# Performance work log

Measured on AMD Instinct MI355X. Metric: run time of the kernel, lower is better.

The kernel has to match this reference:

```python
import jax, jax.numpy as jnp
import numpy as np

EPS_XVAR = 1e-06
EPS_QVAR = 1e-05
EPS_VAR = 1e-05
MIN_SCALE = 0.1  # rbf kernel
EPS_EDGE = 1e-06


def setup_inputs() -> dict:
    key = jax.random.key(0)
    k1, k2, k3, k4 = jax.random.split(key, 4)
    B, O, I, M = 2048, 64, 64, 32
    x = jax.random.normal(k1, (B, I), dtype=jnp.float32)
    # inducing locations: linspace(-1.5, 1.5, M) tiled over (O, I)
    z = jnp.broadcast_to(jnp.linspace(-1.5, 1.5, M, dtype=jnp.float32), (O, I, M))
    q_mu = jax.random.normal(k2, (O, I, M), dtype=jnp.float32) * 0.05
    q_log_var = jnp.full((O, I, M), -3.0, dtype=jnp.float32)
    log_scale = jnp.zeros((O, I), dtype=jnp.float32)
    log_variance = jnp.full((O, I), -1.0, dtype=jnp.float32)
    return {"x": x, "z": z, "q_mu": q_mu, "q_log_var": q_log_var,
            "log_scale": log_scale, "log_variance": log_variance}


def reference(x, z, q_mu, q_log_var, log_scale, log_variance):
    # x: [B, I]; params: [O, I, M] or [O, I]
    x_mean = x
    x_var = jnp.zeros_like(x) + EPS_XVAR

    q_var = jnp.maximum(jnp.exp(q_log_var), EPS_QVAR)           # [O, I, M]
    var_kern = jnp.maximum(jnp.exp(log_variance), EPS_VAR)      # [O, I]
    lengthscale = jnp.maximum(jnp.exp(log_scale), MIN_SCALE)    # [O, I]

    x_mu_exp = x_mean[:, None, :, None]        # [B, 1, I, 1]
    x_var_exp = x_var[:, None, :, None]        # [B, 1, I, 1]
    ell_sq = (lengthscale ** 2)[None, :, :, None]  # [1, O, I, 1]
    vk = var_kern[None, :, :, None]            # [1, O, I, 1]

    denom = ell_sq + x_var_exp                 # [B, O, I, 1]
    diff = x_mu_exp - z[None]                  # [B, O, I, M]
    psi_1 = vk * jnp.sqrt(ell_sq / denom) * jnp.exp(-0.5 * diff ** 2 / denom)

    edge_means = jnp.sum(psi_1 * q_mu[None], axis=-1)                      # [B, O, I]
    edge_vars = jnp.sum(psi_1 ** 2 * (q_var + q_mu ** 2)[None], axis=-1)   # [B, O, I]
    edge_vars = jnp.maximum(edge_vars - edge_means ** 2, EPS_EDGE)

    return edge_means.sum(axis=2), edge_vars.sum(axis=2)  # each [B, O]
```

## Files before the change

kernel.cpp:

```cpp
#include <hip/hip_runtime.h>

#define BATCH 2048
#define ODIM 64
#define IDIM 64
#define MDIM 32

static constexpr float LOG2E = 1.4426950408889634f;

#if __has_builtin(__builtin_amdgcn_exp2f)
#define EXP2F(x) __builtin_amdgcn_exp2f(x)
#else
#define EXP2F(x) exp2f(x)
#endif

typedef float v2f __attribute__((ext_vector_type(2)));


__global__ __launch_bounds__(256) void prep_kernel(
    const float* __restrict__ z, const float* __restrict__ q_mu,
    const float* __restrict__ q_log_var, const float* __restrict__ log_scale,
    const float* __restrict__ log_variance,
    float4* __restrict__ cmq, float4* __restrict__ aux)
{
    int qt = blockIdx.x * 256 + threadIdx.x;
    int oi = qt >> 4;
    int k  = qt & 15;
    int g  = oi * MDIM + 2 * k;

    float ls   = log_scale[oi];
    float lv   = log_variance[oi];
    float ell  = fmaxf(expf(ls), 0.1f);
    float ell2 = ell * ell;
    float vk   = fmaxf(expf(lv), 1e-5f);
    float denom = ell2 + 1e-6f;
    float A    = vk * sqrtf(ell2 / denom);
    float a    = -0.5f * LOG2E / denom;

    float qm0 = q_mu[g],     qm1 = q_mu[g + 1];
    float qv0 = fmaxf(expf(q_log_var[g]),     1e-5f);
    float qv1 = fmaxf(expf(q_log_var[g + 1]), 1e-5f);
    float zm0 = z[g],        zm1 = z[g + 1];
    float w0  = exp2f(a * zm0 * zm0);
    float w1  = exp2f(a * zm1 * zm1);

    float4 c;
    c.x = A * qm0 * w0;
    c.y = A * A * (qv0 + qm0 * qm0) * w0 * w0;
    c.z = A * qm1 * w1;
    c.w = A * A * (qv1 + qm1 * qm1) * w1 * w1;
    cmq[qt] = c;

    if (k == 0) {
        float z0 = z[oi * MDIM + 0];
        float z1 = z[oi * MDIM + 1];
        float dz = z1 - z0;
        aux[oi] = make_float4(a, -2.0f * a * z0, -2.0f * a * dz, 0.0f);
    }
}

__global__ __launch_bounds__(512, 8) void gpkan_main_kernel(
    const float* __restrict__ x, const float4* __restrict__ cmq,
    const float4* __restrict__ aux, float* __restrict__ out)
{
    const int o     = blockIdx.x & (ODIM - 1);
    const int btile = blockIdx.x >> 6;
    const int tid   = threadIdx.x;
    const int lane  = tid & 63;
    const int wave  = __builtin_amdgcn_readfirstlane(tid >> 6);
    const int b0    = btile * 128 + 2 * lane;
    const int i0    = wave * 8;

    __shared__ float red[2][8][128];

    const float4* pA = (const float4*)(x + (size_t)b0 * IDIM + i0);
    const float4* pB = (const float4*)(x + (size_t)(b0 + 1) * IDIM + i0);
    float4 a0 = pA[0], a1 = pA[1];
    float4 bb0 = pB[0], bb1 = pB[1];

    v2f xv[8];
    xv[0].x = a0.x; xv[0].y = bb0.x;
    xv[1].x = a0.y; xv[1].y = bb0.y;
    xv[2].x = a0.z; xv[2].y = bb0.z;
    xv[3].x = a0.w; xv[3].y = bb0.w;
    xv[4].x = a1.x; xv[4].y = bb1.x;
    xv[5].x = a1.y; xv[5].y = bb1.y;
    xv[6].x = a1.z; xv[6].y = bb1.z;
    xv[7].x = a1.w; xv[7].y = bb1.w;

    const float4* __restrict__ Cb = cmq + ((size_t)o * IDIM + i0) * 16;
    const float4* __restrict__ Ab = aux + o * IDIM + i0;

    v2f emt = {0.f, 0.f};
    v2f evt = {0.f, 0.f};

    #pragma unroll
    for (int ii = 0; ii < 8; ++ii) {
        const float4 Ax = Ab[ii];
        const v2f x2 = xv[ii];

        v2f e1 = {Ax.x, Ax.x}, e2 = {Ax.y, Ax.y}, rc = {Ax.z, Ax.z};

        v2f t = __builtin_elementwise_fma(e1, x2, e2) * x2;
        v2f Eb;
        Eb.x = EXP2F(t.x); Eb.y = EXP2F(t.y);
        v2f ur = rc * x2;
        v2f rr;
        rr.x = EXP2F(ur.x); rr.y = EXP2F(ur.y);

        v2f s = rr * rr;
        v2f u = s * s;

        v2f Pe = {0.f, 0.f}, Po = {0.f, 0.f};
        v2f Qe = {0.f, 0.f}, Qo = {0.f, 0.f};

        const float4* C = Cb + ii * 16;
        #pragma unroll
        for (int k = 15; k >= 0; --k) {
            float4 c = C[k];
            v2f c1e = {c.x, c.x}, c2e = {c.y, c.y};
            v2f c1o = {c.z, c.z}, c2o = {c.w, c.w};
            Pe = __builtin_elementwise_fma(Pe, s, c1e);
            Po = __builtin_elementwise_fma(Po, s, c1o);
            Qe = __builtin_elementwise_fma(Qe, u, c2e);
            Qo = __builtin_elementwise_fma(Qo, u, c2o);
        }

        v2f P = __builtin_elementwise_fma(rr, Po, Pe);
        v2f Q = __builtin_elementwise_fma(s,  Qo, Qe);

        v2f em_i = Eb * P;
        v2f ev_i = (Eb * Eb) * Q;

        v2f eps = {1e-6f, 1e-6f};
        v2f d   = __builtin_elementwise_fma(-em_i, em_i, ev_i);
        evt += __builtin_elementwise_max(d, eps);
        emt += em_i;
    }

    red[0][wave][2 * lane + 0] = emt.x;
    red[0][wave][2 * lane + 1] = emt.y;
    red[1][wave][2 * lane + 0] = evt.x;
    red[1][wave][2 * lane + 1] = evt.y;
    __syncthreads();

    if (tid < 256) {
        const int sel = tid >> 7;
        const int l   = tid & 127;
        float acc = 0.f;
        #pragma unroll
        for (int w = 0; w < 8; ++w) acc += red[sel][w][l];
        const int bb = btile * 128 + l;
        if (sel == 0) out[bb * ODIM + o] = acc;
        else          out[BATCH * ODIM + bb * ODIM + o] = acc;
    }
}

extern "C" void kernel_launch(void* const* d_in, const int* in_sizes, int n_in,
                              void* d_out, int out_size, void* d_ws, size_t ws_size,
                              hipStream_t stream) {
    const float* x            = (const float*)d_in[0];
    const float* z            = (const float*)d_in[1];
    const float* q_mu         = (const float*)d_in[2];
    const float* q_log_var    = (const float*)d_in[3];
    const float* log_scale    = (const float*)d_in[4];
    const float* log_variance = (const float*)d_in[5];
    float* out = (float*)d_out;

    char* ws = (char*)d_ws;
    float4* cmq = (float4*)ws;
    float4* aux = (float4*)(ws + (size_t)ODIM * IDIM * 16 * sizeof(float4));

    prep_kernel<<<dim3(256), dim3(256), 0, stream>>>(
        z, q_mu, q_log_var, log_scale, log_variance, cmq, aux);
    gpkan_main_kernel<<<dim3((BATCH / 128) * ODIM), dim3(512), 0, stream>>>(
        x, cmq, aux, out);
}
```

Before: 80.79 us.

## Split input dimension across two blocks and combine partial sums with atomics

```diff
diff --git a/kernel.cpp b/kernel.cpp
--- a/kernel.cpp
+++ b/kernel.cpp
@@ -20,9 +20,12 @@
     const float* __restrict__ z, const float* __restrict__ q_mu,
     const float* __restrict__ q_log_var, const float* __restrict__ log_scale,
     const float* __restrict__ log_variance,
-    float4* __restrict__ cmq, float4* __restrict__ aux)
+    float4* __restrict__ cmq, float4* __restrict__ aux, float4* __restrict__ outz)
 {
     int qt = blockIdx.x * 256 + threadIdx.x;
+
+    outz[qt] = make_float4(0.f, 0.f, 0.f, 0.f);
+
     int oi = qt >> 4;
     int k  = qt & 15;
     int g  = oi * MDIM + 2 * k;
@@ -63,29 +66,23 @@
     const float4* __restrict__ aux, float* __restrict__ out)
 {
     const int o     = blockIdx.x & (ODIM - 1);
-    const int btile = blockIdx.x >> 6;
+    const int btile = (blockIdx.x >> 6) & 15;
+    const int ihalf = blockIdx.x >> 10;
     const int tid   = threadIdx.x;
     const int lane  = tid & 63;
     const int wave  = __builtin_amdgcn_readfirstlane(tid >> 6);
     const int b0    = btile * 128 + 2 * lane;
-    const int i0    = wave * 8;
+    const int i0    = ihalf * 32 + wave * 4;
 
     __shared__ float red[2][8][128];
 
-    const float4* pA = (const float4*)(x + (size_t)b0 * IDIM + i0);
-    const float4* pB = (const float4*)(x + (size_t)(b0 + 1) * IDIM + i0);
-    float4 a0 = pA[0], a1 = pA[1];
-    float4 bb0 = pB[0], bb1 = pB[1];
-
-    v2f xv[8];
-    xv[0].x = a0.x; xv[0].y = bb0.x;
-    xv[1].x = a0.y; xv[1].y = bb0.y;
-    xv[2].x = a0.z; xv[2].y = bb0.z;
-    xv[3].x = a0.w; xv[3].y = bb0.w;
-    xv[4].x = a1.x; xv[4].y = bb1.x;
-    xv[5].x = a1.y; xv[5].y = bb1.y;
-    xv[6].x = a1.z; xv[6].y = bb1.z;
-    xv[7].x = a1.w; xv[7].y = bb1.w;
+    const float4 ax = *(const float4*)(x + (size_t)b0 * IDIM + i0);
+    const float4 bx = *(const float4*)(x + (size_t)(b0 + 1) * IDIM + i0);
+    v2f xv[4];
+    xv[0].x = ax.x; xv[0].y = bx.x;
+    xv[1].x = ax.y; xv[1].y = bx.y;
+    xv[2].x = ax.z; xv[2].y = bx.z;
+    xv[3].x = ax.w; xv[3].y = bx.w;
 
     const float4* __restrict__ Cb = cmq + ((size_t)o * IDIM + i0) * 16;
     const float4* __restrict__ Ab = aux + o * IDIM + i0;
@@ -94,7 +91,7 @@
     v2f evt = {0.f, 0.f};
 
     #pragma unroll
-    for (int ii = 0; ii < 8; ++ii) {
+    for (int ii = 0; ii < 4; ++ii) {
         const float4 Ax = Ab[ii];
         const v2f x2 = xv[ii];
 
@@ -150,8 +147,9 @@
         #pragma unroll
         for (int w = 0; w < 8; ++w) acc += red[sel][w][l];
         const int bb = btile * 128 + l;
-        if (sel == 0) out[bb * ODIM + o] = acc;
-        else          out[BATCH * ODIM + bb * ODIM + o] = acc;
+        float* dst = (sel == 0) ? &out[bb * ODIM + o]
+                                : &out[BATCH * ODIM + bb * ODIM + o];
+        atomicAdd(dst, acc);
     }
 }
 
@@ -171,7 +169,7 @@
     float4* aux = (float4*)(ws + (size_t)ODIM * IDIM * 16 * sizeof(float4));
 
     prep_kernel<<<dim3(256), dim3(256), 0, stream>>>(
-        z, q_mu, q_log_var, log_scale, log_variance, cmq, aux);
-    gpkan_main_kernel<<<dim3((BATCH / 128) * ODIM), dim3(512), 0, stream>>>(
+        z, q_mu, q_log_var, log_scale, log_variance, cmq, aux, (float4*)out);
+    gpkan_main_kernel<<<dim3((BATCH / 128) * ODIM * 2), dim3(512), 0, stream>>>(
         x, cmq, aux, out);
 }
```

Result: slower. 96.62 us (+19.6%).
